# Optimization experiments

Measured on AMD Instinct MI355X. Metric: run time of the kernel, lower is better.

## Reference

```python
import jax, jax.numpy as jnp
import numpy as np

B, T, HS, H, R = 4, 2048, 1024, 16, 16
D = HS // H  # 64 head_dim
LOGIT_01 = float(np.log(0.1 / 0.9))    # g_proj bias init
LOGIT_098 = float(np.log(0.98 / 0.02)) # base decay logits init


def _rope_cos_sin(seq_len, dim, base=10000.0):
    half = dim // 2
    inv_freq = 1.0 / (base ** (jnp.arange(half, dtype=jnp.float32) / half))
    freqs = jnp.arange(seq_len, dtype=jnp.float32)[:, None] * inv_freq[None, :]  # [T, half]
    return jnp.cos(freqs), jnp.sin(freqs)


def _apply_rope(x, cos, sin):
    # x: [B,T,H,D] with D even; rotate interleaved pairs over full D
    c = cos[None, :, None, :]
    s = sin[None, :, None, :]
    x1 = x[..., 0::2]
    x2 = x[..., 1::2]
    r1 = x1 * c - x2 * s
    r2 = x1 * s + x2 * c
    return jnp.stack((r1, r2), axis=-1).reshape(x.shape)


def setup_inputs() -> dict:
    key = jax.random.key(0)
    ks = jax.random.split(key, 10)
    def rn(k, shape, s=0.02):
        return jax.random.normal(k, shape, dtype=jnp.float32) * s
    return {
        "x": jax.random.normal(ks[0], (B, T, HS), dtype=jnp.float32),
        "q_w": rn(ks[1], (HS, HS)),
        "k_w": rn(ks[2], (HS, HS)),
        "v_w": rn(ks[3], (HS, HS)),
        "Wq": rn(ks[4], (H, R, D), 0.05),
        "Wk": rn(ks[5], (H, R, D), 0.05),
        "g_w": rn(ks[6], (H * R, HS)),
        "g_b": jnp.full((H * R,), LOGIT_01, dtype=jnp.float32),
        "base_decay_logits": jnp.full((H, R), LOGIT_098, dtype=jnp.float32),
        "out_w": rn(ks[7], (HS, HS)),
        "out_b": jnp.zeros((HS,), dtype=jnp.float32),
        "ln_g": jnp.ones((HS,), dtype=jnp.float32),
        "ln_b": jnp.zeros((HS,), dtype=jnp.float32),
    }


def reference(x, q_w, k_w, v_w, Wq, Wk, g_w, g_b, base_decay_logits,
              out_w, out_b, ln_g, ln_b):
    b, t, hs = x.shape
    h, r, d = Wq.shape
    # qkv projections (torch Linear: x @ W.T)
    q = (x @ q_w.T).reshape(b, t, h, d)
    k = (x @ k_w.T).reshape(b, t, h, d)
    v = (x @ v_w.T).reshape(b, t, h, d)
    # RoPE (dim_rot == head_dim since it is even)
    cos, sin = _rope_cos_sin(t, d)
    q = _apply_rope(q, cos, sin)
    k = _apply_rope(k, cos, sin)
    # low-rank projections
    q_r = jnp.einsum('bthd,hrd->bthr', q, Wq)
    k_r = jnp.einsum('bthd,hrd->bthr', k, Wk)
    # content gates
    g = jax.nn.sigmoid((x @ g_w.T + g_b).reshape(b, t, h, r))
    decay = jax.nn.sigmoid(base_decay_logits)[None, :, :, None]  # [1,H,r,1]
    scale = 1.0 / jnp.sqrt(jnp.asarray(d, dtype=x.dtype))

    def step(M, inp):
        q_t, k_t, v_t, g_t = inp  # [B,H,r], [B,H,r], [B,H,D], [B,H,r]
        M = M * decay + jnp.einsum('bhr,bhd->bhrd', g_t * k_t * scale, v_t)
        y = jnp.einsum('bhr,bhrd->bhd', q_t, M)
        return M, y

    xs = (q_r.transpose(1, 0, 2, 3), k_r.transpose(1, 0, 2, 3),
          v.transpose(1, 0, 2, 3), g.transpose(1, 0, 2, 3))
    M0 = jnp.zeros((b, h, r, d), dtype=x.dtype)
    _, Y = jax.lax.scan(step, M0, xs)  # Y: [T,B,H,D]
    Y = Y.transpose(1, 0, 2, 3).reshape(b, t, hs)
    out = Y @ out_w.T + out_b  # dropout is identity at eval time
    hres = x + out
    mu = jnp.mean(hres, axis=-1, keepdims=True)
    var = jnp.mean((hres - mu) ** 2, axis=-1, keepdims=True)
    return (hres - mu) / jnp.sqrt(var + 1e-5) * ln_g + ln_b
```

## Files before the change

kernel.cpp:

```cpp
#include <hip/hip_runtime.h>
#include <hip/hip_bf16.h>

#define B_ 4
#define T_ 2048
#define HS_ 1024
#define H_ 16
#define R_ 16
#define D_ 64
#define BT_ (B_*T_)
#define NC_ 3328
#define CHUNK_ 64
#define NCHUNK_ (T_/CHUNK_)

typedef __attribute__((ext_vector_type(8))) short short8;
typedef __attribute__((ext_vector_type(4))) float f32x4;

__device__ __forceinline__ float b2f(ushort u){
    union{unsigned int i; float f;} v; v.i = ((unsigned int)u) << 16; return v.f;
}
__device__ __forceinline__ ushort f2b(float f){
    __hip_bfloat16 h = __float2bfloat16(f);
    return *reinterpret_cast<ushort*>(&h);
}
__device__ __forceinline__ float sigm(float x){ return 1.f/(1.f+expf(-x)); }

__device__ __forceinline__ void gl_lds16(const void* g, void* l){
    __builtin_amdgcn_global_load_lds((const __attribute__((address_space(1))) void*)g,
                                     (__attribute__((address_space(3))) void*)l,
                                     16, 0, 0);
}

__global__ void k_prep(const float* __restrict__ x,
                       const float* __restrict__ qw, const float* __restrict__ kw,
                       const float* __restrict__ vw, const float* __restrict__ gw,
                       const float* __restrict__ outw,
                       ushort* __restrict__ xbf, ushort* __restrict__ wcat,
                       ushort* __restrict__ owbf,
                       float* __restrict__ cosT, float* __restrict__ sinT){
    int bid = blockIdx.x;
    if(bid < 8192){
        int i = bid*256 + threadIdx.x;
        float4 v = ((const float4*)x)[i];
        ushort4 o; o.x=f2b(v.x); o.y=f2b(v.y); o.z=f2b(v.z); o.w=f2b(v.w);
        ((ushort4*)xbf)[i] = o;
    } else if(bid < 11520){
        int i = (bid-8192)*256 + threadIdx.x;
        int e = i*4;
        int row = e >> 10, col = e & 1023;
        const float* src;
        if      (row < 1024) src = qw + (size_t)row*1024 + col;
        else if (row < 2048) src = kw + (size_t)(row-1024)*1024 + col;
        else if (row < 3072) src = vw + (size_t)(row-2048)*1024 + col;
        else                 src = gw + (size_t)(row-3072)*1024 + col;
        float4 v = *(const float4*)src;
        ushort4 o; o.x=f2b(v.x); o.y=f2b(v.y); o.z=f2b(v.z); o.w=f2b(v.w);
        ((ushort4*)wcat)[i] = o;
    } else if(bid < 12544){
        int i = (bid-11520)*256 + threadIdx.x;
        float4 v = ((const float4*)outw)[i];
        ushort4 o; o.x=f2b(v.x); o.y=f2b(v.y); o.z=f2b(v.z); o.w=f2b(v.w);
        ((ushort4*)owbf)[i] = o;
    } else {
        int i = (bid-12544)*256 + threadIdx.x;
        int t = i >> 5, f = i & 31;
        float inv = powf(10000.f, -(float)f/32.f);
        float a = (float)t * inv;
        cosT[i] = cosf(a);
        sinT[i] = sinf(a);
    }
}

__global__ __launch_bounds__(512, 4) void k_gemm256d(const ushort* __restrict__ A,
                                                     const ushort* __restrict__ Bm,
                                                     ushort* __restrict__ C,
                                                     int K, int ldc){
    __shared__ __align__(16) ushort lds[24576];
    const int tid  = threadIdx.x;
    const int lane = tid & 63, w = tid >> 6;
    const int fr = lane & 15, fg = lane >> 4;
    const int wm = w >> 1, wn = w & 1;
    const int qa = ((fg + (fr >> 1)) & 3) * 8;

    int mt = gridDim.x;
    int L = blockIdx.y * mt + blockIdx.x;
    int bxi, byi;
    int msub = mt >> 3;
    if((mt & 7) == 0 && msub > 0){
        int xcd = L & 7, c = L >> 3;
        bxi = xcd * msub + (c % msub);
        byi = c / msub;
    } else { bxi = blockIdx.x; byi = blockIdx.y; }
    const long arow0 = (long)bxi * 256;
    const long brow0 = (long)byi * 128;

    const int srow = tid >> 2;
    const int scol = ((((tid & 3) - (tid >> 3)) & 3)) * 8;
    const ushort* gsrc0 = A  + (arow0 +       srow) * (size_t)K + scol;
    const ushort* gsrc1 = A  + (arow0 + 128 + srow) * (size_t)K + scol;
    const ushort* gsrc2 = Bm + (brow0 +       srow) * (size_t)K + scol;

#define STG(t) do{ ushort* _b = &lds[((t)&1)*12288 + w*512];                  \
    gl_lds16(gsrc0 + (size_t)(t)*32, _b);                                     \
    gl_lds16(gsrc1 + (size_t)(t)*32, _b + 4096);                              \
    gl_lds16(gsrc2 + (size_t)(t)*32, _b + 8192); }while(0)

    f32x4 acc[4][4];
#pragma unroll
    for(int m=0;m<4;m++)
#pragma unroll
        for(int n=0;n<4;n++)
            acc[m][n] = (f32x4){0.f,0.f,0.f,0.f};

    const int NT = K >> 5;
    STG(0);
    for(int t=0; t<NT; ++t){
        asm volatile("s_waitcnt vmcnt(0)" ::: "memory");
        __builtin_amdgcn_s_barrier();
        __builtin_amdgcn_sched_barrier(0);
        if(t+1 < NT) STG(t+1);
        const int sb = (t&1)*12288;
        short8 af[4], bv[4];
#pragma unroll
        for(int mm=0; mm<4; ++mm)
            af[mm] = *(const short8*)&lds[sb + (wm*64 + mm*16 + fr)*32 + qa];
#pragma unroll
        for(int nf=0; nf<4; ++nf)
            bv[nf] = *(const short8*)&lds[sb + 8192 + (wn*64 + nf*16 + fr)*32 + qa];
        __builtin_amdgcn_s_setprio(1);
#pragma unroll
        for(int mm=0; mm<4; ++mm)
#pragma unroll
        for(int nf=0; nf<4; ++nf)
            acc[mm][nf] = __builtin_amdgcn_mfma_f32_16x16x32_bf16(
                af[mm], bv[nf], acc[mm][nf], 0,0,0);
        __builtin_amdgcn_s_setprio(0);
    }
#undef STG

#pragma unroll
    for(int m=0;m<4;m++)
#pragma unroll
        for(int n=0;n<4;n++){
            long col = brow0 + wn*64 + n*16 + fr;
#pragma unroll
            for(int j=0;j<4;j++){
                long row = arow0 + wm*64 + m*16 + fg*4 + j;
                C[row*(size_t)ldc + col] = f2b(acc[m][n][j]);
            }
        }
}

__global__ __launch_bounds__(256) void k_rope_proj(const ushort* __restrict__ qkvg,
                                                   const float* __restrict__ cosT,
                                                   const float* __restrict__ sinT,
                                                   const float* __restrict__ Wq,
                                                   const float* __restrict__ Wk,
                                                   const float* __restrict__ gb,
                                                   float* __restrict__ qr_s,
                                                   float* __restrict__ gk_s){
    __shared__ __align__(16) ushort lq[64*72], lk[64*72];
    __shared__ __align__(16) ushort wql[16*72], wkl[16*72];
    int tid = threadIdx.x, wid = tid >> 6, lane = tid & 63;
    int bt0 = blockIdx.x * 64;
    int h   = blockIdx.y;

    {
        int row = tid >> 4, seg = tid & 15;
        float4 wq4 = *(const float4*)(Wq + (size_t)h*1024 + row*64 + seg*4);
        float4 wk4 = *(const float4*)(Wk + (size_t)h*1024 + row*64 + seg*4);
        ushort* dq = &wql[row*72 + seg*4];
        ushort* dk = &wkl[row*72 + seg*4];
        dq[0]=f2b(wq4.x); dq[1]=f2b(wq4.y); dq[2]=f2b(wq4.z); dq[3]=f2b(wq4.w);
        dk[0]=f2b(wk4.x); dk[1]=f2b(wk4.y); dk[2]=f2b(wk4.z); dk[3]=f2b(wk4.w);
    }

#pragma unroll
    for(int rep=0; rep<2; ++rep){
        int flat = rep*256 + tid;
        int row = flat >> 3, seg = flat & 7;
        int t = (bt0 + row) & 2047;
        const ushort* base = qkvg + (size_t)(bt0+row)*NC_ + h*64 + seg*8;
        short8 q8 = *(const short8*)base;
        short8 k8 = *(const short8*)(base + 1024);
        float4 cv = *(const float4*)&cosT[t*32 + seg*4];
        float4 sv = *(const float4*)&sinT[t*32 + seg*4];
        float qf[8], kf[8];
#pragma unroll
        for(int j=0;j<8;j++){ qf[j]=b2f((ushort)q8[j]); kf[j]=b2f((ushort)k8[j]); }
        float c4[4] = {cv.x,cv.y,cv.z,cv.w};
        float s4[4] = {sv.x,sv.y,sv.z,sv.w};
        short8 qo, ko;
#pragma unroll
        for(int p=0;p<4;p++){
            float c=c4[p], s=s4[p];
            qo[2*p]   = (short)f2b(qf[2*p]*c - qf[2*p+1]*s);
            qo[2*p+1] = (short)f2b(qf[2*p]*s + qf[2*p+1]*c);
            ko[2*p]   = (short)f2b(kf[2*p]*c - kf[2*p+1]*s);
            ko[2*p+1] = (short)f2b(kf[2*p]*s + kf[2*p+1]*c);
        }
        *(short8*)&lq[row*72 + seg*8] = qo;
        *(short8*)&lk[row*72 + seg*8] = ko;
    }
    __syncthreads();

    int fr = lane & 15, fg = lane >> 4;
    int wrow = wid*16;
    short8 aq0 = *(const short8*)&lq[(wrow+fr)*72 + fg*8];
    short8 aq1 = *(const short8*)&lq[(wrow+fr)*72 + 32 + fg*8];
    short8 ak0 = *(const short8*)&lk[(wrow+fr)*72 + fg*8];
    short8 ak1 = *(const short8*)&lk[(wrow+fr)*72 + 32 + fg*8];
    short8 bq0 = *(const short8*)&wql[fr*72 + fg*8];
    short8 bq1 = *(const short8*)&wql[fr*72 + 32 + fg*8];
    short8 bk0 = *(const short8*)&wkl[fr*72 + fg*8];
    short8 bk1 = *(const short8*)&wkl[fr*72 + 32 + fg*8];
    f32x4 accq = (f32x4){0.f,0.f,0.f,0.f};
    f32x4 acck = (f32x4){0.f,0.f,0.f,0.f};
    accq = __builtin_amdgcn_mfma_f32_16x16x32_bf16(aq0, bq0, accq, 0,0,0);
    accq = __builtin_amdgcn_mfma_f32_16x16x32_bf16(aq1, bq1, accq, 0,0,0);
    acck = __builtin_amdgcn_mfma_f32_16x16x32_bf16(ak0, bk0, acck, 0,0,0);
    acck = __builtin_amdgcn_mfma_f32_16x16x32_bf16(ak1, bk1, acck, 0,0,0);

    int r = fr;
    float gbv = gb[h*16 + r];
#pragma unroll
    for(int j=0;j<4;j++){
        int bt = bt0 + wrow + fg*4 + j;
        int t  = bt & 2047, b = bt >> 11;
        size_t o = (((size_t)(b*16 + h))*2048 + t)*16 + r;
        qr_s[o] = accq[j];
        float gl = b2f(qkvg[(size_t)bt*NC_ + 3072 + h*16 + r]) + gbv;
        gk_s[o] = sigm(gl) * acck[j] * 0.125f;
    }
}

__global__ __launch_bounds__(64) void k_scan_local(const ushort* __restrict__ qkvg,
                                                   const float* __restrict__ gk_s,
                                                   const float* __restrict__ bdl,
                                                   float* __restrict__ Mloc){
    int lane = threadIdx.x;
    int bx = blockIdx.x;
    int ch = bx & (NCHUNK_-1), bh = bx >> 5;
    int b = bh >> 4, h = bh & 15;
    float dec[16], M[16];
#pragma unroll
    for(int r=0;r<16;r++){ dec[r] = sigm(bdl[h*16+r]); M[r] = 0.f; }

    int t0 = ch*CHUNK_;
    const float4*  gk4 = (const float4*)(gk_s + (((size_t)bh)*2048 + t0)*16);
    const ushort*  vp  = qkvg + ((size_t)(b*2048 + t0))*NC_ + 2048 + h*64 + lane;
    for(int tt=0; tt<CHUNK_; ++tt){
        float v = b2f(*vp); vp += NC_;
        float4 a0 = gk4[0], a1 = gk4[1], a2 = gk4[2], a3 = gk4[3]; gk4 += 4;
        float gk[16] = {a0.x,a0.y,a0.z,a0.w, a1.x,a1.y,a1.z,a1.w,
                        a2.x,a2.y,a2.z,a2.w, a3.x,a3.y,a3.z,a3.w};
#pragma unroll
        for(int r=0;r<16;r++) M[r] = fmaf(M[r], dec[r], gk[r]*v);
    }
    float* mp = Mloc + ((size_t)bx)*1024 + lane;
#pragma unroll
    for(int r=0;r<16;r++) mp[r*64] = M[r];
}

__global__ __launch_bounds__(64) void k_scan_carry(float* __restrict__ Mloc,
                                                   const float* __restrict__ bdl){
    int lane = threadIdx.x;
    int sub = blockIdx.x & 3, bh = blockIdx.x >> 2, h = bh & 15;
    float decC[4], S[4];
#pragma unroll
    for(int rr=0;rr<4;rr++){
        decC[rr] = powf(sigm(bdl[h*16 + sub*4 + rr]), (float)CHUNK_);
        S[rr] = 0.f;
    }
    for(int c=0;c<NCHUNK_;c++){
        float* p = Mloc + ((size_t)(bh*NCHUNK_ + c))*1024 + lane + sub*4*64;
#pragma unroll
        for(int rr=0;rr<4;rr++){
            float m = p[rr*64];
            p[rr*64] = S[rr];
            S[rr] = fmaf(S[rr], decC[rr], m);
        }
    }
}

__global__ __launch_bounds__(64) void k_scan_out(const ushort* __restrict__ qkvg,
                                                 const float* __restrict__ gk_s,
                                                 const float* __restrict__ qr_s,
                                                 const float* __restrict__ Mst,
                                                 const float* __restrict__ bdl,
                                                 ushort* __restrict__ Ybf){
    int lane = threadIdx.x;
    int bx = blockIdx.x;
    int ch = bx & (NCHUNK_-1), bh = bx >> 5;
    int b = bh >> 4, h = bh & 15;
    float dec[16], M[16];
#pragma unroll
    for(int r=0;r<16;r++) dec[r] = sigm(bdl[h*16+r]);
    const float* sp = Mst + ((size_t)bx)*1024 + lane;
#pragma unroll
    for(int r=0;r<16;r++) M[r] = sp[r*64];

    int t0 = ch*CHUNK_;
    const float4* gk4 = (const float4*)(gk_s + (((size_t)bh)*2048 + t0)*16);
    const float4* q4  = (const float4*)(qr_s + (((size_t)bh)*2048 + t0)*16);
    const ushort* vp  = qkvg + ((size_t)(b*2048 + t0))*NC_ + 2048 + h*64 + lane;
    ushort*       yp  = Ybf  + ((size_t)(b*2048 + t0))*1024 + h*64 + lane;
    for(int tt=0; tt<CHUNK_; ++tt){
        float v = b2f(*vp); vp += NC_;
        float4 a0 = gk4[0], a1 = gk4[1], a2 = gk4[2], a3 = gk4[3]; gk4 += 4;
        float4 b0 = q4[0],  b1 = q4[1],  b2 = q4[2],  b3 = q4[3];  q4  += 4;
        float gk[16] = {a0.x,a0.y,a0.z,a0.w, a1.x,a1.y,a1.z,a1.w,
                        a2.x,a2.y,a2.z,a2.w, a3.x,a3.y,a3.z,a3.w};
        float qv[16] = {b0.x,b0.y,b0.z,b0.w, b1.x,b1.y,b1.z,b1.w,
                        b2.x,b2.y,b2.z,b2.w, b3.x,b3.y,b3.z,b3.w};
        float y = 0.f;
#pragma unroll
        for(int r=0;r<16;r++){
            M[r] = fmaf(M[r], dec[r], gk[r]*v);
            y    = fmaf(qv[r], M[r], y);
        }
        *yp = f2b(y); yp += 1024;
    }
}

__global__ __launch_bounds__(256) void k_ln(const float* __restrict__ x,
                                            const ushort* __restrict__ O,
                                            const float* __restrict__ ob,
                                            const float* __restrict__ lg,
                                            const float* __restrict__ lb,
                                            float* __restrict__ out){
    __shared__ float red[8];
    int row = blockIdx.x, tid = threadIdx.x;
    float hv[4];
    float sum = 0.f, ssq = 0.f;
#pragma unroll
    for(int k2=0;k2<4;k2++){
        int j = tid + k2*256;
        float v = x[(size_t)row*1024 + j] + b2f(O[(size_t)row*1024 + j]) + ob[j];
        hv[k2] = v; sum += v; ssq += v*v;
    }
#pragma unroll
    for(int off=32; off; off >>= 1){
        sum += __shfl_down(sum, off, 64);
        ssq += __shfl_down(ssq, off, 64);
    }
    int wid = tid >> 6, lane = tid & 63;
    if(lane == 0){ red[wid] = sum; red[4+wid] = ssq; }
    __syncthreads();
    if(tid == 0){
        float s = red[0]+red[1]+red[2]+red[3];
        float q = red[4]+red[5]+red[6]+red[7];
        float mu = s / 1024.f;
        red[0] = mu;
        red[1] = q / 1024.f - mu*mu;
    }
    __syncthreads();
    float mu = red[0];
    float inv = rsqrtf(red[1] + 1e-5f);
#pragma unroll
    for(int k2=0;k2<4;k2++){
        int j = tid + k2*256;
        out[(size_t)row*1024 + j] = (hv[k2]-mu)*inv*lg[j] + lb[j];
    }
}

extern "C" void kernel_launch(void* const* d_in, const int* in_sizes, int n_in,
                              void* d_out, int out_size, void* d_ws, size_t ws_size,
                              hipStream_t stream){
    const float* x    = (const float*)d_in[0];
    const float* q_w  = (const float*)d_in[1];
    const float* k_w  = (const float*)d_in[2];
    const float* v_w  = (const float*)d_in[3];
    const float* Wq   = (const float*)d_in[4];
    const float* Wk   = (const float*)d_in[5];
    const float* g_w  = (const float*)d_in[6];
    const float* g_b  = (const float*)d_in[7];
    const float* bdl  = (const float*)d_in[8];
    const float* outw = (const float*)d_in[9];
    const float* outb = (const float*)d_in[10];
    const float* ln_g = (const float*)d_in[11];
    const float* ln_b = (const float*)d_in[12];
    float* out = (float*)d_out;

    char* ws = (char*)d_ws;
    size_t off = 0;
    ushort* xbf  = (ushort*)(ws + off); off += (size_t)BT_*HS_*2;
    ushort* wcat = (ushort*)(ws + off); off += (size_t)NC_*HS_*2;
    ushort* owbf = (ushort*)(ws + off); off += (size_t)HS_*HS_*2;
    float*  cosT = (float*)(ws + off);  off += (size_t)T_*32*4;
    float*  sinT = (float*)(ws + off);  off += (size_t)T_*32*4;
    ushort* qkvg = (ushort*)(ws + off); off += (size_t)BT_*NC_*2;
    float*  qr_s = (float*)(ws + off);  off += (size_t)BT_*H_*R_*4;
    float*  gk_s = (float*)(ws + off);  off += (size_t)BT_*H_*R_*4;
    float*  Mloc = (float*)(ws + off);  off += (size_t)B_*H_*NCHUNK_*R_*D_*4;
    ushort* Ybf = xbf;
    ushort* O   = qkvg;

    k_prep<<<12800, 256, 0, stream>>>(x, q_w, k_w, v_w, g_w, outw,
                                      xbf, wcat, owbf, cosT, sinT);

    k_gemm256d<<<dim3(BT_/256, NC_/128), 512, 0, stream>>>(xbf, wcat, qkvg, HS_, NC_);

    k_rope_proj<<<dim3(BT_/64, H_), 256, 0, stream>>>(qkvg, cosT, sinT, Wq, Wk, g_b, qr_s, gk_s);

    k_scan_local<<<B_*H_*NCHUNK_, 64, 0, stream>>>(qkvg, gk_s, bdl, Mloc);
    k_scan_carry<<<B_*H_*4, 64, 0, stream>>>(Mloc, bdl);
    k_scan_out<<<B_*H_*NCHUNK_, 64, 0, stream>>>(qkvg, gk_s, qr_s, Mloc, bdl, Ybf);

    k_gemm256d<<<dim3(BT_/256, HS_/128), 512, 0, stream>>>(Ybf, owbf, O, HS_, HS_);

    k_ln<<<BT_, 256, 0, stream>>>(x, O, outb, ln_g, ln_b, out);

    (void)in_sizes; (void)n_in; (void)out_size; (void)ws_size;
}
```

Before: 192.1 us.

## Replace GEMM with 256x256 tile, four-stage LDS pipeline and split half-tile MFMA

Both bf16 GEMMs now use a kernel with a 256x256 output tile (8 waves in a 2x4 layout, 32 accumulators per wave) instead of 256x128. The kernel keeps a 4-deep ring of LDS stages with three tiles prefetched, and each k-step is split into two halves whose global-to-LDS loads interleave with MFMA work under explicit barriers and waitcnts. The goal is more data reuse per loaded tile and better hiding of memory latency behind compute. The cost is 128KB of LDS and more registers per block, which lowers occupancy, and fewer blocks in the grid (for example 32x4 for the output projection), which may leave CUs underused.

```diff
diff --git a/kernel.cpp b/kernel.cpp
--- a/kernel.cpp
+++ b/kernel.cpp
@@ -70,15 +70,15 @@
     }
 }
 
-__global__ __launch_bounds__(512, 4) void k_gemm256d(const ushort* __restrict__ A,
-                                                     const ushort* __restrict__ Bm,
-                                                     ushort* __restrict__ C,
-                                                     int K, int ldc){
-    __shared__ __align__(16) ushort lds[24576];
+__global__ __launch_bounds__(512, 2) void k_gemm8p(const ushort* __restrict__ A,
+                                                   const ushort* __restrict__ Bm,
+                                                   ushort* __restrict__ C,
+                                                   int K, int ldc){
+    __shared__ __align__(16) ushort lds[65536];
     const int tid  = threadIdx.x;
     const int lane = tid & 63, w = tid >> 6;
     const int fr = lane & 15, fg = lane >> 4;
-    const int wm = w >> 1, wn = w & 1;
+    const int wm = w >> 2, wn = w & 3;
     const int qa = ((fg + (fr >> 1)) & 3) * 8;
 
     int mt = gridDim.x;
@@ -91,60 +91,86 @@
         byi = c / msub;
     } else { bxi = blockIdx.x; byi = blockIdx.y; }
     const long arow0 = (long)bxi * 256;
-    const long brow0 = (long)byi * 128;
+    const long brow0 = (long)byi * 256;
 
     const int srow = tid >> 2;
     const int scol = ((((tid & 3) - (tid >> 3)) & 3)) * 8;
-    const ushort* gsrc0 = A  + (arow0 +       srow) * (size_t)K + scol;
-    const ushort* gsrc1 = A  + (arow0 + 128 + srow) * (size_t)K + scol;
-    const ushort* gsrc2 = Bm + (brow0 +       srow) * (size_t)K + scol;
-
-#define STG(t) do{ ushort* _b = &lds[((t)&1)*12288 + w*512];                  \
-    gl_lds16(gsrc0 + (size_t)(t)*32, _b);                                     \
-    gl_lds16(gsrc1 + (size_t)(t)*32, _b + 4096);                              \
-    gl_lds16(gsrc2 + (size_t)(t)*32, _b + 8192); }while(0)
-
-    f32x4 acc[4][4];
-#pragma unroll
-    for(int m=0;m<4;m++)
+    const ushort* gs0 = A  + (arow0 +       srow) * (size_t)K + scol;
+    const ushort* gs1 = A  + (arow0 + 128 + srow) * (size_t)K + scol;
+    const ushort* gs2 = Bm + (brow0 +       srow) * (size_t)K + scol;
+    const ushort* gs3 = Bm + (brow0 + 128 + srow) * (size_t)K + scol;
+    const int NT = K >> 5;
+
+#define STG2(s, h) do{ int _ss = (s) < NT ? (s) : NT-1;                       \
+    ushort* _b = &lds[((s)&3)*16384 + (h)*8192 + w*512];                      \
+    if((h)==0){ gl_lds16(gs0 + (size_t)_ss*32, _b);                           \
+                gl_lds16(gs1 + (size_t)_ss*32, _b + 4096); }                  \
+    else      { gl_lds16(gs2 + (size_t)_ss*32, _b);                           \
+                gl_lds16(gs3 + (size_t)_ss*32, _b + 4096); } }while(0)
+#define RDAF(dst, s, h) _Pragma("unroll") for(int mm=0;mm<4;++mm){            \
+    int _r = wm*128 + (h)*64 + mm*16 + fr;                                    \
+    dst[mm] = *(const short8*)&lds[((s)&3)*16384 + _r*32 + qa]; }
+#define RDBV(dst, s) _Pragma("unroll") for(int nf=0;nf<4;++nf){               \
+    int _r = wn*64 + nf*16 + fr;                                              \
+    dst[nf] = *(const short8*)&lds[((s)&3)*16384 + 8192 + _r*32 + qa]; }
+#define MFMA16(mh, afx) do{ __builtin_amdgcn_s_setprio(1);                    \
+    _Pragma("unroll") for(int mm=0;mm<4;++mm)                                 \
+    _Pragma("unroll") for(int nf=0;nf<4;++nf)                                 \
+        acc[(mh)*4+mm][nf] = __builtin_amdgcn_mfma_f32_16x16x32_bf16(         \
+            afx[mm], bv[nf], acc[(mh)*4+mm][nf], 0,0,0);                      \
+    __builtin_amdgcn_s_setprio(0); }while(0)
+
+    f32x4 acc[8][4];
+#pragma unroll
+    for(int m=0;m<8;m++)
 #pragma unroll
         for(int n=0;n<4;n++)
             acc[m][n] = (f32x4){0.f,0.f,0.f,0.f};
 
-    const int NT = K >> 5;
-    STG(0);
-    for(int t=0; t<NT; ++t){
-        asm volatile("s_waitcnt vmcnt(0)" ::: "memory");
+    STG2(0,0); STG2(0,1); STG2(1,0); STG2(1,1); STG2(2,0); STG2(2,1);
+    asm volatile("s_waitcnt vmcnt(8)" ::: "memory");
+    __builtin_amdgcn_s_barrier();
+    __builtin_amdgcn_sched_barrier(0);
+
+    short8 af0[4], af1[4], bv[4];
+    for(int s=0; s<NT; ++s){
+        RDAF(af0, s, 0);
+        RDBV(bv, s);
+        STG2(s+3, 0);
+        __builtin_amdgcn_sched_barrier(0);
         __builtin_amdgcn_s_barrier();
-        __builtin_amdgcn_sched_barrier(0);
-        if(t+1 < NT) STG(t+1);
-        const int sb = (t&1)*12288;
-        short8 af[4], bv[4];
-#pragma unroll
-        for(int mm=0; mm<4; ++mm)
-            af[mm] = *(const short8*)&lds[sb + (wm*64 + mm*16 + fr)*32 + qa];
-#pragma unroll
-        for(int nf=0; nf<4; ++nf)
-            bv[nf] = *(const short8*)&lds[sb + 8192 + (wn*64 + nf*16 + fr)*32 + qa];
-        __builtin_amdgcn_s_setprio(1);
-#pragma unroll
-        for(int mm=0; mm<4; ++mm)
-#pragma unroll
-        for(int nf=0; nf<4; ++nf)
-            acc[mm][nf] = __builtin_amdgcn_mfma_f32_16x16x32_bf16(
-                af[mm], bv[nf], acc[mm][nf], 0,0,0);
-        __builtin_amdgcn_s_setprio(0);
-    }
-#undef STG
-
-#pragma unroll
-    for(int m=0;m<4;m++)
+        asm volatile("s_waitcnt lgkmcnt(0)" ::: "memory");
+        __builtin_amdgcn_sched_barrier(0);
+        MFMA16(0, af0);
+        __builtin_amdgcn_sched_barrier(0);
+        __builtin_amdgcn_s_barrier();
+        __builtin_amdgcn_sched_barrier(0);
+        RDAF(af1, s, 1);
+        STG2(s+3, 1);
+        asm volatile("s_waitcnt vmcnt(8)" ::: "memory");
+        __builtin_amdgcn_sched_barrier(0);
+        __builtin_amdgcn_s_barrier();
+        asm volatile("s_waitcnt lgkmcnt(0)" ::: "memory");
+        __builtin_amdgcn_sched_barrier(0);
+        MFMA16(1, af1);
+        __builtin_amdgcn_sched_barrier(0);
+        __builtin_amdgcn_s_barrier();
+        __builtin_amdgcn_sched_barrier(0);
+    }
+    asm volatile("s_waitcnt vmcnt(0)" ::: "memory");
+#undef STG2
+#undef RDAF
+#undef RDBV
+#undef MFMA16
+
+#pragma unroll
+    for(int m=0;m<8;m++)
 #pragma unroll
         for(int n=0;n<4;n++){
             long col = brow0 + wn*64 + n*16 + fr;
 #pragma unroll
             for(int j=0;j<4;j++){
-                long row = arow0 + wm*64 + m*16 + fg*4 + j;
+                long row = arow0 + wm*128 + (m>>2)*64 + (m&3)*16 + fg*4 + j;
                 C[row*(size_t)ldc + col] = f2b(acc[m][n][j]);
             }
         }
@@ -398,7 +424,7 @@
     k_prep<<<12800, 256, 0, stream>>>(x, q_w, k_w, v_w, g_w, outw,
                                       xbf, wcat, owbf, cosT, sinT);
 
-    k_gemm256d<<<dim3(BT_/256, NC_/128), 512, 0, stream>>>(xbf, wcat, qkvg, HS_, NC_);
+    k_gemm8p<<<dim3(BT_/256, NC_/256), 512, 0, stream>>>(xbf, wcat, qkvg, HS_, NC_);
 
     k_rope_proj<<<dim3(BT_/64, H_), 256, 0, stream>>>(qkvg, cosT, sinT, Wq, Wk, g_b, qr_s, gk_s);
 
@@ -406,7 +432,7 @@
     k_scan_carry<<<B_*H_*4, 64, 0, stream>>>(Mloc, bdl);
     k_scan_out<<<B_*H_*NCHUNK_, 64, 0, stream>>>(qkvg, gk_s, qr_s, Mloc, bdl, Ybf);
 
-    k_gemm256d<<<dim3(BT_/256, HS_/128), 512, 0, stream>>>(Ybf, owbf, O, HS_, HS_);
+    k_gemm8p<<<dim3(BT_/256, HS_/256), 512, 0, stream>>>(Ybf, owbf, O, HS_, HS_);
 
     k_ln<<<BT_, 256, 0, stream>>>(x, O, outb, ln_g, ln_b, out);
 
```

Result: slower. 199.8 us (+4.0%).

## Fuse chunked scan local, carry and output kernels into one block per head

Applied to the files above, without the earlier changes.

The three scan kernels (per-chunk local state, cross-chunk carry, output replay) become one kernel with one 1024-thread block per (batch, head). Per-chunk states live in a 128KB LDS array instead of a global Mloc buffer, and grid-wide sync points become __syncthreads. This removes two launches and the global round trip of the chunk states. In exchange the grid shrinks from 2048 small blocks to 64 large ones, so only a fraction of the CUs are used and each wave handles two chunks in sequence.

```diff
diff --git a/kernel.cpp b/kernel.cpp
--- a/kernel.cpp
+++ b/kernel.cpp
@@ -233,92 +233,81 @@
     }
 }
 
-__global__ __launch_bounds__(64) void k_scan_local(const ushort* __restrict__ qkvg,
-                                                   const float* __restrict__ gk_s,
-                                                   const float* __restrict__ bdl,
-                                                   float* __restrict__ Mloc){
-    int lane = threadIdx.x;
-    int bx = blockIdx.x;
-    int ch = bx & (NCHUNK_-1), bh = bx >> 5;
+__global__ __launch_bounds__(1024) void k_scan_fused(const ushort* __restrict__ qkvg,
+                                                     const float* __restrict__ gk_s,
+                                                     const float* __restrict__ qr_s,
+                                                     const float* __restrict__ bdl,
+                                                     ushort* __restrict__ Ybf){
+    __shared__ float Ml[NCHUNK_*1024];
+    int bh = blockIdx.x;
     int b = bh >> 4, h = bh & 15;
-    float dec[16], M[16];
-#pragma unroll
-    for(int r=0;r<16;r++){ dec[r] = sigm(bdl[h*16+r]); M[r] = 0.f; }
-
-    int t0 = ch*CHUNK_;
-    const float4*  gk4 = (const float4*)(gk_s + (((size_t)bh)*2048 + t0)*16);
-    const ushort*  vp  = qkvg + ((size_t)(b*2048 + t0))*NC_ + 2048 + h*64 + lane;
-    for(int tt=0; tt<CHUNK_; ++tt){
-        float v = b2f(*vp); vp += NC_;
-        float4 a0 = gk4[0], a1 = gk4[1], a2 = gk4[2], a3 = gk4[3]; gk4 += 4;
-        float gk[16] = {a0.x,a0.y,a0.z,a0.w, a1.x,a1.y,a1.z,a1.w,
-                        a2.x,a2.y,a2.z,a2.w, a3.x,a3.y,a3.z,a3.w};
-#pragma unroll
-        for(int r=0;r<16;r++) M[r] = fmaf(M[r], dec[r], gk[r]*v);
-    }
-    float* mp = Mloc + ((size_t)bx)*1024 + lane;
-#pragma unroll
-    for(int r=0;r<16;r++) mp[r*64] = M[r];
-}
-
-__global__ __launch_bounds__(64) void k_scan_carry(float* __restrict__ Mloc,
-                                                   const float* __restrict__ bdl){
-    int lane = threadIdx.x;
-    int sub = blockIdx.x & 3, bh = blockIdx.x >> 2, h = bh & 15;
-    float decC[4], S[4];
-#pragma unroll
-    for(int rr=0;rr<4;rr++){
-        decC[rr] = powf(sigm(bdl[h*16 + sub*4 + rr]), (float)CHUNK_);
-        S[rr] = 0.f;
-    }
-    for(int c=0;c<NCHUNK_;c++){
-        float* p = Mloc + ((size_t)(bh*NCHUNK_ + c))*1024 + lane + sub*4*64;
-#pragma unroll
-        for(int rr=0;rr<4;rr++){
-            float m = p[rr*64];
-            p[rr*64] = S[rr];
-            S[rr] = fmaf(S[rr], decC[rr], m);
+    int tid = threadIdx.x, wid = tid >> 6, lane = tid & 63;
+    float dec[16];
+#pragma unroll
+    for(int r=0;r<16;r++) dec[r] = sigm(bdl[h*16+r]);
+
+#pragma unroll
+    for(int cc=0; cc<2; ++cc){
+        int ch = wid*2 + cc;
+        int t0 = ch*CHUNK_;
+        const float4*  gk4 = (const float4*)(gk_s + (((size_t)bh)*2048 + t0)*16);
+        const ushort*  vp  = qkvg + ((size_t)(b*2048 + t0))*NC_ + 2048 + h*64 + lane;
+        float M[16];
+#pragma unroll
+        for(int r=0;r<16;r++) M[r] = 0.f;
+        for(int tt=0; tt<CHUNK_; ++tt){
+            float v = b2f(*vp); vp += NC_;
+            float4 a0 = gk4[0], a1 = gk4[1], a2 = gk4[2], a3 = gk4[3]; gk4 += 4;
+            float gk[16] = {a0.x,a0.y,a0.z,a0.w, a1.x,a1.y,a1.z,a1.w,
+                            a2.x,a2.y,a2.z,a2.w, a3.x,a3.y,a3.z,a3.w};
+#pragma unroll
+            for(int r=0;r<16;r++) M[r] = fmaf(M[r], dec[r], gk[r]*v);
         }
-    }
-}
-
-__global__ __launch_bounds__(64) void k_scan_out(const ushort* __restrict__ qkvg,
-                                                 const float* __restrict__ gk_s,
-                                                 const float* __restrict__ qr_s,
-                                                 const float* __restrict__ Mst,
-                                                 const float* __restrict__ bdl,
-                                                 ushort* __restrict__ Ybf){
-    int lane = threadIdx.x;
-    int bx = blockIdx.x;
-    int ch = bx & (NCHUNK_-1), bh = bx >> 5;
-    int b = bh >> 4, h = bh & 15;
-    float dec[16], M[16];
-#pragma unroll
-    for(int r=0;r<16;r++) dec[r] = sigm(bdl[h*16+r]);
-    const float* sp = Mst + ((size_t)bx)*1024 + lane;
-#pragma unroll
-    for(int r=0;r<16;r++) M[r] = sp[r*64];
-
-    int t0 = ch*CHUNK_;
-    const float4* gk4 = (const float4*)(gk_s + (((size_t)bh)*2048 + t0)*16);
-    const float4* q4  = (const float4*)(qr_s + (((size_t)bh)*2048 + t0)*16);
-    const ushort* vp  = qkvg + ((size_t)(b*2048 + t0))*NC_ + 2048 + h*64 + lane;
-    ushort*       yp  = Ybf  + ((size_t)(b*2048 + t0))*1024 + h*64 + lane;
-    for(int tt=0; tt<CHUNK_; ++tt){
-        float v = b2f(*vp); vp += NC_;
-        float4 a0 = gk4[0], a1 = gk4[1], a2 = gk4[2], a3 = gk4[3]; gk4 += 4;
-        float4 b0 = q4[0],  b1 = q4[1],  b2 = q4[2],  b3 = q4[3];  q4  += 4;
-        float gk[16] = {a0.x,a0.y,a0.z,a0.w, a1.x,a1.y,a1.z,a1.w,
-                        a2.x,a2.y,a2.z,a2.w, a3.x,a3.y,a3.z,a3.w};
-        float qv[16] = {b0.x,b0.y,b0.z,b0.w, b1.x,b1.y,b1.z,b1.w,
-                        b2.x,b2.y,b2.z,b2.w, b3.x,b3.y,b3.z,b3.w};
-        float y = 0.f;
-#pragma unroll
-        for(int r=0;r<16;r++){
-            M[r] = fmaf(M[r], dec[r], gk[r]*v);
-            y    = fmaf(qv[r], M[r], y);
+        float* mp = &Ml[ch*1024 + lane];
+#pragma unroll
+        for(int r=0;r<16;r++) mp[r*64] = M[r];
+    }
+    __syncthreads();
+
+    {
+        float dc = powf(dec[tid >> 6], (float)CHUNK_);
+        float S = 0.f;
+        for(int c=0; c<NCHUNK_; ++c){
+            float m = Ml[c*1024 + tid];
+            Ml[c*1024 + tid] = S;
+            S = fmaf(S, dc, m);
         }
-        *yp = f2b(y); yp += 1024;
+    }
+    __syncthreads();
+
+#pragma unroll
+    for(int cc=0; cc<2; ++cc){
+        int ch = wid*2 + cc;
+        int t0 = ch*CHUNK_;
+        float M[16];
+        const float* sp = &Ml[ch*1024 + lane];
+#pragma unroll
+        for(int r=0;r<16;r++) M[r] = sp[r*64];
+        const float4* gk4 = (const float4*)(gk_s + (((size_t)bh)*2048 + t0)*16);
+        const float4* q4  = (const float4*)(qr_s + (((size_t)bh)*2048 + t0)*16);
+        const ushort* vp  = qkvg + ((size_t)(b*2048 + t0))*NC_ + 2048 + h*64 + lane;
+        ushort*       yp  = Ybf  + ((size_t)(b*2048 + t0))*1024 + h*64 + lane;
+        for(int tt=0; tt<CHUNK_; ++tt){
+            float v = b2f(*vp); vp += NC_;
+            float4 a0 = gk4[0], a1 = gk4[1], a2 = gk4[2], a3 = gk4[3]; gk4 += 4;
+            float4 b0 = q4[0],  b1 = q4[1],  b2 = q4[2],  b3 = q4[3];  q4  += 4;
+            float gk[16] = {a0.x,a0.y,a0.z,a0.w, a1.x,a1.y,a1.z,a1.w,
+                            a2.x,a2.y,a2.z,a2.w, a3.x,a3.y,a3.z,a3.w};
+            float qv[16] = {b0.x,b0.y,b0.z,b0.w, b1.x,b1.y,b1.z,b1.w,
+                            b2.x,b2.y,b2.z,b2.w, b3.x,b3.y,b3.z,b3.w};
+            float y = 0.f;
+#pragma unroll
+            for(int r=0;r<16;r++){
+                M[r] = fmaf(M[r], dec[r], gk[r]*v);
+                y    = fmaf(qv[r], M[r], y);
+            }
+            *yp = f2b(y); yp += 1024;
+        }
     }
 }
 
@@ -391,7 +380,6 @@
     ushort* qkvg = (ushort*)(ws + off); off += (size_t)BT_*NC_*2;
     float*  qr_s = (float*)(ws + off);  off += (size_t)BT_*H_*R_*4;
     float*  gk_s = (float*)(ws + off);  off += (size_t)BT_*H_*R_*4;
-    float*  Mloc = (float*)(ws + off);  off += (size_t)B_*H_*NCHUNK_*R_*D_*4;
     ushort* Ybf = xbf;
     ushort* O   = qkvg;
 
@@ -402,9 +390,7 @@
 
     k_rope_proj<<<dim3(BT_/64, H_), 256, 0, stream>>>(qkvg, cosT, sinT, Wq, Wk, g_b, qr_s, gk_s);
 
-    k_scan_local<<<B_*H_*NCHUNK_, 64, 0, stream>>>(qkvg, gk_s, bdl, Mloc);
-    k_scan_carry<<<B_*H_*4, 64, 0, stream>>>(Mloc, bdl);
-    k_scan_out<<<B_*H_*NCHUNK_, 64, 0, stream>>>(qkvg, gk_s, qr_s, Mloc, bdl, Ybf);
+    k_scan_fused<<<B_*H_, 1024, 0, stream>>>(qkvg, gk_s, qr_s, bdl, Ybf);
 
     k_gemm256d<<<dim3(BT_/256, HS_/128), 512, 0, stream>>>(Ybf, owbf, O, HS_, HS_);
 
```

Result: slower. 313.1 us (+63.0%).
